# Kernel tuning notes

Hardware: AMD Instinct MI355X
Metric: run time of the kernel (lower is better)

Reference implementation:

```python
import jax, jax.numpy as jnp
import numpy as np

N = 100000   # nodes
E = 1600000  # edges per relation
D = 128      # feature dim (dim_in == dim_out)
H = 128      # semantic-attention hidden size
R = 3        # relations


def setup_inputs() -> dict:
    key = jax.random.key(0)
    ks = jax.random.split(key, 16)
    inp = {"x": jax.random.normal(ks[0], (N, D), jnp.float32)}
    for r in range(R):
        inp[f"src{r}"] = jax.random.randint(ks[1 + 2 * r], (E,), 0, N)
        inp[f"dst{r}"] = jax.random.randint(ks[2 + 2 * r], (E,), 0, N)
        inp[f"W{r}"] = jax.random.normal(ks[7 + r], (D, D), jnp.float32) / np.sqrt(D)
    inp["aW"] = jax.random.normal(ks[10], (D, H), jnp.float32) / np.sqrt(D)
    inp["ab"] = jnp.zeros((H,), jnp.float32)
    inp["aq"] = jax.random.normal(ks[11], (H,), jnp.float32) / np.sqrt(H)
    return inp


def _gcn_rel(x, W, src, dst):
    # DGL GraphConv with norm='both', no bias:
    # out = D_in^{-1/2} . A . D_out^{-1/2} . X . W   (degrees clamped to >= 1)
    ones = jnp.ones(src.shape, dtype=x.dtype)
    deg_out = jnp.maximum(jax.ops.segment_sum(ones, src, num_segments=N), 1.0)
    deg_in = jnp.maximum(jax.ops.segment_sum(ones, dst, num_segments=N), 1.0)
    h = (x @ W) * jax.lax.rsqrt(deg_out)[:, None]          # (N, D)
    agg = jax.ops.segment_sum(h[src], dst, num_segments=N)  # gather->scatter (E, D)
    return agg * jax.lax.rsqrt(deg_in)[:, None]


def reference(x, W0, W1, W2, aW, ab, aq, src0, dst0, src1, dst1, src2, dst2):
    # per-relation message passing, stacked over relation axis: (N, R, D)
    z = jnp.stack([
        _gcn_rel(x, W0, src0, dst0),
        _gcn_rel(x, W1, src1, dst1),
        _gcn_rel(x, W2, src2, dst2),
    ], axis=1)
    # SemanticAttention: w_r = mean_n( tanh(z W1 + b) @ q );  beta = softmax(w)
    proj = jnp.tanh(jnp.einsum('nrd,dh->nrh', z, aW) + ab)   # (N, R, H)
    w = jnp.einsum('nrh,h->r', proj, aq) / z.shape[0]        # (R,)
    beta = jax.nn.softmax(w)
    return jnp.einsum('nrd,r->nd', z, beta)                  # (N, D)
```

## Files before the change

kernel.cpp:

```cpp
#include <hip/hip_runtime.h>
#include <hip/hip_bf16.h>

#define NN 100000
#define EE 1600000
#define DD 128
#define RNG 8
#define RSZ 12500
#define CAPR 16
#define CHK 32

typedef __attribute__((ext_vector_type(8))) short bf16x8;
typedef __attribute__((ext_vector_type(4))) float f32x4;
union FB { unsigned u[4]; uint4 u4; bf16x8 v; };

__device__ inline unsigned f2bf(float x){unsigned u=__float_as_uint(x);return (u+0x7fffu+((u>>16)&1u))>>16;}
__device__ inline unsigned bf16pack(float a,float b){return (f2bf(b)<<16)|(f2bf(a)&0xffffu);}
__device__ inline unsigned packsplit(float v){unsigned hb=f2bf(v);float hf=__uint_as_float(hb<<16);unsigned lb=f2bf(v-hf);return (hb<<16)|(lb&0xffffu);}
__device__ inline float bflo(unsigned u){return __uint_as_float(u<<16);}
__device__ inline float bfhi(unsigned u){return __uint_as_float(u&0xffff0000u);}

struct Bufs {
  const float* x;
  const int *s0,*d0,*s1,*d1,*s2,*d2;
  const float *W0,*W1,*W2,*aW,*ab,*aq;
  unsigned *h0,*h1,*h2;
  unsigned *zb0,*zb1,*zb2;
  ushort *csr0,*csr1;
  int *cursor;
  float *wpart;
  float *wblk;
  float *rs;
  int *histpart;
  ushort *fhi,*flo;
  float *out;
};

__global__ __launch_bounds__(256) void k0_kernel(Bufs B) {
  __shared__ unsigned bins[RSZ/2];
  int b = blockIdx.x;
  if (b < 768) {
    int range = b & 7, chunk = (b >> 3) & 31, rel = b >> 8;
    const int* src = rel==0?B.s0: rel==1?B.s1:B.s2;
    for (int i=threadIdx.x;i<RSZ/2;i+=256) bins[i]=0;
    __syncthreads();
    int lo = range*RSZ, e0 = chunk*(EE/CHK);
    for (int e=e0+(int)threadIdx.x; e<e0+EE/CHK; e+=256){
      int v = src[e]-lo;
      if ((unsigned)v<(unsigned)RSZ) atomicAdd(&bins[v>>1], 1u<<((v&1)*16));
    }
    __syncthreads();
    int* outp = B.histpart + ((size_t)(rel*CHK+chunk))*NN + lo;
    for (int i=threadIdx.x;i<RSZ;i+=256) outp[i] = (bins[i>>1]>>((i&1)*16)) & 0xffff;
  } else if (b < 768+587) {
    int id = b-768;
    const int Z = 3*NN*RNG + 4;
    int* dst = B.cursor;
#pragma unroll
    for (int k=0;k<4;++k){
      int off = id*4096 + k*1024 + (int)threadIdx.x*4;
      if (off+4 <= Z) *(int4*)(dst+off) = make_int4(0,0,0,0);
      else { for (int j=0;j<4;++j) if (off+j<Z) dst[off+j]=0; }
    }
  } else {
    int m = b - (768+587);
    const float* W = m==0?B.W0: m==1?B.W1: m==2?B.W2: B.aW;
    ushort* ho = B.fhi + (size_t)m*16384;
    ushort* lp = B.flo + (size_t)m*16384;
    for (int idx=threadIdx.x; idx<16384; idx+=256){
      int j=idx&7, lane=(idx>>3)&63, ft=(idx>>9)&7, ks=idx>>12;
      int k = ks*32 + (lane>>4)*8 + j;
      int f = ft*16 + (lane&15);
      float v = W[k*128+f];
      unsigned hb = f2bf(v);
      float hf = __uint_as_float(hb<<16);
      ho[idx]=(ushort)hb; lp[idx]=(ushort)f2bf(v-hf);
    }
  }
}

__device__ inline void do_bucket(int id, int rel, const Bufs& B) {
  const int* src = rel==0?B.s0: rel==1?B.s1:B.s2;
  const int* dst = rel==0?B.d0: rel==1?B.d1:B.d2;
  int* cur = B.cursor + (size_t)rel*NN*RNG;
  ushort* csr = (rel==1)? B.csr1 : B.csr0;
  int e0 = id*512;
  for (int e=e0+(int)threadIdx.x; e<e0+512; e+=256){
    int s = src[e], d = dst[e];
    int rg = s / RSZ;
    int pos = atomicAdd(&cur[d*RNG+rg], 1);
    if (pos < CAPR) csr[((size_t)d*RNG+rg)*CAPR + pos] = (ushort)(s - rg*RSZ);
  }
}

__device__ inline void do_reduce(int id, const Bufs& B) {
  int tid = id*256 + threadIdx.x;
  if (tid >= 3*NN) return;
  int rel = tid/NN, n = tid-rel*NN;
  const int* p = B.histpart + (size_t)rel*CHK*NN + n;
  int s = 0;
#pragma unroll
  for (int c=0;c<CHK;++c) s += p[(size_t)c*NN];
  B.rs[tid] = rsqrtf(fmaxf((float)s, 1.f));
}

__device__ inline void do_gemm0(int tile, int rel, const Bufs& B, unsigned (*As)[132]) {
  const uint4* Bhi = (const uint4*)(B.fhi + (size_t)rel*16384);
  const uint4* Blo = (const uint4*)(B.flo + (size_t)rel*16384);
  unsigned* h = rel==0?B.h0: rel==1?B.h1:B.h2;
  int t = threadIdx.x, row0 = tile*32;
  for (int idx=t; idx<32*32; idx+=256){
    int r = idx>>5, c4 = (idx&31)<<2;
    float4 v = *(const float4*)(B.x + (size_t)(row0+r)*DD + c4);
    uint4 pk; pk.x=packsplit(v.x); pk.y=packsplit(v.y); pk.z=packsplit(v.z); pk.w=packsplit(v.w);
    *(uint4*)&As[r][c4] = pk;
  }
  __syncthreads();
  int wv=t>>6, l=t&63, ln=l&15, lk=l>>4;
  int nrow=(wv&1)*16+ln, fh=wv>>1;
  f32x4 acc[4];
#pragma unroll
  for (int i=0;i<4;++i) acc[i] = (f32x4){0.f,0.f,0.f,0.f};
#pragma unroll
  for (int ks=0;ks<4;++ks){
    unsigned u[8];
    int kd = ks*32 + lk*8;
    *(uint4*)&u[0] = *(const uint4*)&As[nrow][kd];
    *(uint4*)&u[4] = *(const uint4*)&As[nrow][kd+4];
    FB bh, bl;
#pragma unroll
    for (int i=0;i<4;++i){
      bh.u[i] = (u[2*i]>>16) | (u[2*i+1]&0xffff0000u);
      bl.u[i] = (u[2*i]&0xffffu) | (u[2*i+1]<<16);
    }
#pragma unroll
    for (int fi=0;fi<4;++fi){
      int ft = fh*4+fi;
      FB wh, wl;
      wh.u4 = Bhi[(ks*8+ft)*64 + l];
      wl.u4 = Blo[(ks*8+ft)*64 + l];
      acc[fi] = __builtin_amdgcn_mfma_f32_16x16x32_bf16(wh.v, bh.v, acc[fi],0,0,0);
      acc[fi] = __builtin_amdgcn_mfma_f32_16x16x32_bf16(wl.v, bh.v, acc[fi],0,0,0);
      acc[fi] = __builtin_amdgcn_mfma_f32_16x16x32_bf16(wh.v, bl.v, acc[fi],0,0,0);
    }
  }
  int node = row0+nrow;
#pragma unroll
  for (int fi=0;fi<4;++fi){
    int ft = fh*4+fi;
    uint2 o;
    o.x = bf16pack(acc[fi][0], acc[fi][1]);
    o.y = bf16pack(acc[fi][2], acc[fi][3]);
    *(uint2*)(h + (size_t)node*64 + ft*8 + lk*2) = o;
  }
}

__device__ inline void do_gather(int id, int rel, const Bufs& B) {
  int node = id*4 + (threadIdx.x>>6);
  int lane = threadIdx.x & 63;
  const int* cur = B.cursor + (size_t)rel*NN*RNG + (size_t)node*RNG;
  const ushort* csr = (rel==1)? B.csr1 : B.csr0;
  const unsigned* h = rel==0?B.h0: rel==1?B.h1:B.h2;
  int cnt[RNG];
  int deg = 0, maxc = 0;
#pragma unroll
  for (int k=0;k<RNG;++k){
    int c = cur[k];
    deg += c;
    c = min(c, CAPR);
    cnt[k] = c;
    maxc = max(maxc, c);
  }
  const ushort* base = csr + (size_t)node*(RNG*CAPR);
  float ax = 0.f, ay = 0.f;
  for (int s=0;s<maxc;++s){
    unsigned u[RNG];
#pragma unroll
    for (int k=0;k<RNG;++k){
      if (s < cnt[k]){
        int idx = k*RSZ + (int)base[k*CAPR + s];
        u[k] = h[(size_t)idx*64 + lane];
      }
    }
#pragma unroll
    for (int k=0;k<RNG;++k){
      if (s < cnt[k]){ ax += bflo(u[k]); ay += bfhi(u[k]); }
    }
  }
  float sc = rsqrtf(fmaxf((float)deg, 1.f));
  unsigned* zb = rel==0?B.zb0: rel==1?B.zb1:B.zb2;
  zb[(size_t)node*64+lane] = bf16pack(ax*sc, ay*sc);
}

__device__ inline void do_g1b(int tile, int rel, const Bufs& B,
                              unsigned (*As)[68], float* red) {
  const unsigned* zb = rel==0?B.zb0: rel==1?B.zb1:B.zb2;
  const uint4* Bhi = (const uint4*)(B.fhi + (size_t)3*16384);
  const uint4* Blo = (const uint4*)(B.flo + (size_t)3*16384);
  int t = threadIdx.x, row0 = tile*32;
  for (int idx=t; idx<32*16; idx+=256){
    int r = idx>>4, c4 = (idx&15)<<2;
    *(uint4*)&As[r][c4] = *(const uint4*)(zb + (size_t)(row0+r)*64 + c4);
  }
  __syncthreads();
  int wv=t>>6, l=t&63, ln=l&15, lk=l>>4;
  int nrow=(wv&1)*16+ln, fh=wv>>1;
  f32x4 acc[4];
#pragma unroll
  for (int i=0;i<4;++i) acc[i] = (f32x4){0.f,0.f,0.f,0.f};
#pragma unroll
  for (int ks=0;ks<4;++ks){
    FB bb; bb.u4 = *(const uint4*)&As[nrow][ks*16 + lk*4];
#pragma unroll
    for (int fi=0;fi<4;++fi){
      int ft = fh*4+fi;
      FB wh, wl;
      wh.u4 = Bhi[(ks*8+ft)*64 + l];
      wl.u4 = Blo[(ks*8+ft)*64 + l];
      acc[fi] = __builtin_amdgcn_mfma_f32_16x16x32_bf16(wh.v, bb.v, acc[fi],0,0,0);
      acc[fi] = __builtin_amdgcn_mfma_f32_16x16x32_bf16(wl.v, bb.v, acc[fi],0,0,0);
    }
  }
  float s = 0.f;
#pragma unroll
  for (int fi=0;fi<4;++fi){
#pragma unroll
    for (int r=0;r<4;++r){
      int f = (fh*4+fi)*16 + lk*4 + r;
      float v = acc[fi][r] + B.ab[f];
      float e = __expf(2.f*v);
      s += (1.f - 2.f/(e+1.f)) * B.aq[f];
    }
  }
#pragma unroll
  for (int m=1;m<64;m<<=1) s += __shfl_xor(s, m);
  if (l==0) red[wv] = s;
  __syncthreads();
  if (t==0) B.wblk[rel*3125 + tile] = red[0]+red[1]+red[2]+red[3];
}

__device__ inline void do_hscale(int aidx, const Bufs& B) {
  int gn = aidx >> 4;
  float f = B.rs[gn];
  uint4* h4 = (uint4*)B.h0;
  uint4 u = h4[aidx];
  u.x = bf16pack(bflo(u.x)*f, bfhi(u.x)*f);
  u.y = bf16pack(bflo(u.y)*f, bfhi(u.y)*f);
  u.z = bf16pack(bflo(u.z)*f, bfhi(u.z)*f);
  u.w = bf16pack(bflo(u.w)*f, bfhi(u.w)*f);
  h4[aidx] = u;
}


__global__ __launch_bounds__(256) void megaA(Bufs B) {
  __shared__ unsigned As[32][132];
  const int n0=3125, n1=9375;
  const int tot = n0+n1+1172;
  int b = blockIdx.x;
  long f = ((long)b*n0)/tot;
  if (((long)(b+1)*n0)/tot > f){ do_bucket((int)f, 0, B); return; }
  int b1 = b-(int)f; int tt = tot-n0;
  f = ((long)b1*n1)/tt;
  if (((long)(b1+1)*n1)/tt > f){ int g=(int)f; do_gemm0(g%3125, g/3125, B, As); return; }
  do_reduce(b1-(int)f, B);
}

__global__ __launch_bounds__(256) void hscaleA_kernel(Bufs B) {
  do_hscale(blockIdx.x*256 + threadIdx.x, B);
}

__global__ __launch_bounds__(256) void megaGBH(Bufs B) {
  const int n0=25000, n1=3125;
  const int tot = n0+n1+12500;
  int b = blockIdx.x;
  long f = ((long)b*n0)/tot;
  if (((long)(b+1)*n0)/tot > f){ do_gather((int)f, 0, B); return; }
  int b1 = b-(int)f; int tt = tot-n0;
  f = ((long)b1*n1)/tt;
  if (((long)(b1+1)*n1)/tt > f){ do_bucket((int)f, 1, B); return; }
  do_hscale(NN*16 + (b1-(int)f)*256 + (int)threadIdx.x, B);
}

__global__ __launch_bounds__(256) void megaGB(Bufs B) {
  const int n0=25000, n1=3125;
  const int tot = n0+n1;
  int b = blockIdx.x;
  long f = ((long)b*n0)/tot;
  if (((long)(b+1)*n0)/tot > f) do_gather((int)f, 1, B);
  else                          do_bucket(b-(int)f, 2, B);
}

__global__ __launch_bounds__(256) void megaG(Bufs B) {
  do_gather(blockIdx.x, 2, B);
}

__global__ __launch_bounds__(256) void megaC(Bufs B) {
  __shared__ unsigned As[32][68];
  __shared__ float red[4];
  int b = blockIdx.x;
  if (b < 3125)      do_g1b(b, 0, B, As, red);
  else if (b < 6250) do_g1b(b-3125, 1, B, As, red);
  else               do_g1b(b-6250, 2, B, As, red);
}

__global__ __launch_bounds__(256) void wreduce_kernel(Bufs B) {
  __shared__ float red[4];
  int rel = blockIdx.x;
  const float* p = B.wblk + rel*3125;
  float s = 0.f;
  for (int i = threadIdx.x; i < 3125; i += 256) s += p[i];
#pragma unroll
  for (int m=1;m<64;m<<=1) s += __shfl_xor(s, m);
  int wv = threadIdx.x>>6, l = threadIdx.x&63;
  if (l==0) red[wv] = s;
  __syncthreads();
  if (threadIdx.x==0) B.wpart[rel] = red[0]+red[1]+red[2]+red[3];
}

__global__ __launch_bounds__(256) void combine_kernel(Bufs B) {
  int tid = blockIdx.x*256 + threadIdx.x;
  float w0 = B.wpart[0]*(1.f/NN), w1 = B.wpart[1]*(1.f/NN), w2 = B.wpart[2]*(1.f/NN);
  float m = fmaxf(w0, fmaxf(w1,w2));
  float e0 = expf(w0-m), e1 = expf(w1-m), e2 = expf(w2-m);
  float inv = 1.f/(e0+e1+e2);
  float b0 = e0*inv, b1 = e1*inv, b2 = e2*inv;
  unsigned u0 = B.zb0[tid], u1 = B.zb1[tid], u2 = B.zb2[tid];
  float2 o;
  o.x = b0*bflo(u0) + b1*bflo(u1) + b2*bflo(u2);
  o.y = b0*bfhi(u0) + b1*bfhi(u1) + b2*bfhi(u2);
  ((float2*)B.out)[tid] = o;
}

extern "C" void kernel_launch(void* const* d_in, const int* in_sizes, int n_in,
                              void* d_out, int out_size, void* d_ws, size_t ws_size,
                              hipStream_t stream) {
  Bufs B;
  B.x  = (const float*)d_in[0];
  B.s0 = (const int*)d_in[1]; B.d0 = (const int*)d_in[2]; B.W0 = (const float*)d_in[3];
  B.s1 = (const int*)d_in[4]; B.d1 = (const int*)d_in[5]; B.W1 = (const float*)d_in[6];
  B.s2 = (const int*)d_in[7]; B.d2 = (const int*)d_in[8]; B.W2 = (const float*)d_in[9];
  B.aW = (const float*)d_in[10]; B.ab = (const float*)d_in[11]; B.aq = (const float*)d_in[12];
  B.out = (float*)d_out;

  char* p = (char*)d_ws;
  auto alloc = [&](size_t bytes){ char* r = p; p += (bytes + 255) & ~(size_t)255; return r; };
  B.zb0 = (unsigned*)alloc((size_t)NN*64*4);
  B.zb1 = (unsigned*)alloc((size_t)NN*64*4);
  B.h0  = (unsigned*)alloc((size_t)NN*64*4);
  B.h1  = (unsigned*)alloc((size_t)NN*64*4);
  B.h2  = (unsigned*)alloc((size_t)NN*64*4);
  B.csr0 = (ushort*)alloc((size_t)NN*RNG*CAPR*2);
  B.csr1 = (ushort*)alloc((size_t)NN*RNG*CAPR*2);
  B.cursor = (int*)alloc(((size_t)3*NN*RNG + 4)*4);
  B.wpart  = (float*)(B.cursor + (size_t)3*NN*RNG);
  B.wblk = (float*)alloc((size_t)3*3125*4);
  B.rs  = (float*)alloc((size_t)3*NN*4);
  B.fhi = (ushort*)alloc((size_t)4*16384*2);
  B.flo = (ushort*)alloc((size_t)4*16384*2);
  B.histpart = (int*)B.zb0;
  B.zb2 = B.h0;

  k0_kernel<<<1359, 256, 0, stream>>>(B);
  megaA<<<3125+9375+1172, 256, 0, stream>>>(B);
  hscaleA_kernel<<<NN*16/256, 256, 0, stream>>>(B);
  megaGBH<<<25000+3125+12500, 256, 0, stream>>>(B);
  megaGB<<<25000+3125, 256, 0, stream>>>(B);
  megaG<<<25000, 256, 0, stream>>>(B);
  megaC<<<3125+3125+3125, 256, 0, stream>>>(B);
  wreduce_kernel<<<3, 256, 0, stream>>>(B);
  combine_kernel<<<(NN*64)/256, 256, 0, stream>>>(B);
}
```

Measured before the change: 771.5 us.

## Move relation-0 bucketing into first kernel and zero cursors with memset

The cursor-zeroing blocks leave the first kernel and become a hipMemsetAsync. Relation-0 edge bucketing moves from megaA into a new first kernel, megaK0, where it runs alongside the degree histogram and weight-split prep. megaA now holds only the GEMM and reduce blocks. The aim is to balance work across launches and shorten the critical path, at the cost of an extra memset operation on the stream.

```diff
diff --git a/kernel.cpp b/kernel.cpp
--- a/kernel.cpp
+++ b/kernel.cpp
@@ -35,46 +35,33 @@
   float *out;
 };
 
-__global__ __launch_bounds__(256) void k0_kernel(Bufs B) {
-  __shared__ unsigned bins[RSZ/2];
-  int b = blockIdx.x;
-  if (b < 768) {
-    int range = b & 7, chunk = (b >> 3) & 31, rel = b >> 8;
-    const int* src = rel==0?B.s0: rel==1?B.s1:B.s2;
-    for (int i=threadIdx.x;i<RSZ/2;i+=256) bins[i]=0;
-    __syncthreads();
-    int lo = range*RSZ, e0 = chunk*(EE/CHK);
-    for (int e=e0+(int)threadIdx.x; e<e0+EE/CHK; e+=256){
-      int v = src[e]-lo;
-      if ((unsigned)v<(unsigned)RSZ) atomicAdd(&bins[v>>1], 1u<<((v&1)*16));
-    }
-    __syncthreads();
-    int* outp = B.histpart + ((size_t)(rel*CHK+chunk))*NN + lo;
-    for (int i=threadIdx.x;i<RSZ;i+=256) outp[i] = (bins[i>>1]>>((i&1)*16)) & 0xffff;
-  } else if (b < 768+587) {
-    int id = b-768;
-    const int Z = 3*NN*RNG + 4;
-    int* dst = B.cursor;
-#pragma unroll
-    for (int k=0;k<4;++k){
-      int off = id*4096 + k*1024 + (int)threadIdx.x*4;
-      if (off+4 <= Z) *(int4*)(dst+off) = make_int4(0,0,0,0);
-      else { for (int j=0;j<4;++j) if (off+j<Z) dst[off+j]=0; }
-    }
-  } else {
-    int m = b - (768+587);
-    const float* W = m==0?B.W0: m==1?B.W1: m==2?B.W2: B.aW;
-    ushort* ho = B.fhi + (size_t)m*16384;
-    ushort* lp = B.flo + (size_t)m*16384;
-    for (int idx=threadIdx.x; idx<16384; idx+=256){
-      int j=idx&7, lane=(idx>>3)&63, ft=(idx>>9)&7, ks=idx>>12;
-      int k = ks*32 + (lane>>4)*8 + j;
-      int f = ft*16 + (lane&15);
-      float v = W[k*128+f];
-      unsigned hb = f2bf(v);
-      float hf = __uint_as_float(hb<<16);
-      ho[idx]=(ushort)hb; lp[idx]=(ushort)f2bf(v-hf);
-    }
+__device__ inline void do_hist(int hid, const Bufs& B, unsigned* bins) {
+  int range = hid & 7, chunk = (hid >> 3) & 31, rel = hid >> 8;
+  const int* src = rel==0?B.s0: rel==1?B.s1:B.s2;
+  for (int i=threadIdx.x;i<RSZ/2;i+=256) bins[i]=0;
+  __syncthreads();
+  int lo = range*RSZ, e0 = chunk*(EE/CHK);
+  for (int e=e0+(int)threadIdx.x; e<e0+EE/CHK; e+=256){
+    int v = src[e]-lo;
+    if ((unsigned)v<(unsigned)RSZ) atomicAdd(&bins[v>>1], 1u<<((v&1)*16));
+  }
+  __syncthreads();
+  int* outp = B.histpart + ((size_t)(rel*CHK+chunk))*NN + lo;
+  for (int i=threadIdx.x;i<RSZ;i+=256) outp[i] = (bins[i>>1]>>((i&1)*16)) & 0xffff;
+}
+
+__device__ inline void do_prep(int m, const Bufs& B) {
+  const float* W = m==0?B.W0: m==1?B.W1: m==2?B.W2: B.aW;
+  ushort* ho = B.fhi + (size_t)m*16384;
+  ushort* lp = B.flo + (size_t)m*16384;
+  for (int idx=threadIdx.x; idx<16384; idx+=256){
+    int j=idx&7, lane=(idx>>3)&63, ft=(idx>>9)&7, ks=idx>>12;
+    int k = ks*32 + (lane>>4)*8 + j;
+    int f = ft*16 + (lane&15);
+    float v = W[k*128+f];
+    unsigned hb = f2bf(v);
+    float hf = __uint_as_float(hb<<16);
+    ho[idx]=(ushort)hb; lp[idx]=(ushort)f2bf(v-hf);
   }
 }
 
@@ -251,17 +238,26 @@
 }
 
 
+__global__ __launch_bounds__(256) void megaK0(Bufs B) {
+  __shared__ unsigned bins[RSZ/2];
+  const int n0=3125, n1=772;
+  const int tot = n0+n1;
+  int b = blockIdx.x;
+  long f = ((long)b*n0)/tot;
+  if (((long)(b+1)*n0)/tot > f){ do_bucket((int)f, 0, B); return; }
+  int hid = b-(int)f;
+  if (hid < 768) do_hist(hid, B, bins);
+  else           do_prep(hid-768, B);
+}
+
 __global__ __launch_bounds__(256) void megaA(Bufs B) {
   __shared__ unsigned As[32][132];
-  const int n0=3125, n1=9375;
-  const int tot = n0+n1+1172;
+  const int n0=9375;
+  const int tot = n0+1172;
   int b = blockIdx.x;
   long f = ((long)b*n0)/tot;
-  if (((long)(b+1)*n0)/tot > f){ do_bucket((int)f, 0, B); return; }
-  int b1 = b-(int)f; int tt = tot-n0;
-  f = ((long)b1*n1)/tt;
-  if (((long)(b1+1)*n1)/tt > f){ int g=(int)f; do_gemm0(g%3125, g/3125, B, As); return; }
-  do_reduce(b1-(int)f, B);
+  if (((long)(b+1)*n0)/tot > f){ int g=(int)f; do_gemm0(g%3125, g/3125, B, As); return; }
+  do_reduce(b-(int)f, B);
 }
 
 __global__ __launch_bounds__(256) void hscaleA_kernel(Bufs B) {
@@ -359,8 +355,9 @@
   B.histpart = (int*)B.zb0;
   B.zb2 = B.h0;
 
-  k0_kernel<<<1359, 256, 0, stream>>>(B);
-  megaA<<<3125+9375+1172, 256, 0, stream>>>(B);
+  hipMemsetAsync(B.cursor, 0, ((size_t)3*NN*RNG + 4)*4, stream);
+  megaK0<<<3125+772, 256, 0, stream>>>(B);
+  megaA<<<9375+1172, 256, 0, stream>>>(B);
   hscaleA_kernel<<<NN*16/256, 256, 0, stream>>>(B);
   megaGBH<<<25000+3125+12500, 256, 0, stream>>>(B);
   megaGB<<<25000+3125, 256, 0, stream>>>(B);
```

After: 783.3 us. About the same (+1.5%).
